# Kernel optimization log

Hardware: AMD Instinct MI355X
Metric: run time of the kernel (lower is better)

Reference implementation:

```python
import jax, jax.numpy as jnp
import numpy as np

EPS = 1e-8  # torch.nn.CosineSimilarity default eps


def setup_inputs() -> dict:
    key = jax.random.key(0)
    ks = jax.random.split(key, 7)
    B, T, D = 2048, 128, 128
    x = jax.random.normal(ks[0], (B, T, D), dtype=jnp.float32)
    def lin(k, fan_out, fan_in):
        kw, kb = jax.random.split(k)
        bound = 1.0 / np.sqrt(fan_in)
        W = jax.random.uniform(kw, (fan_out, fan_in), minval=-bound, maxval=bound, dtype=jnp.float32)
        b = jax.random.uniform(kb, (fan_out,), minval=-bound, maxval=bound, dtype=jnp.float32)
        return W, b
    W1, b1 = lin(ks[1], 96, 128)
    W2, b2 = lin(ks[2], 72, 96)
    W3, b3 = lin(ks[3], 64, 72)
    return {"x": x, "W1": W1, "b1": b1, "W2": W2, "b2": b2, "W3": W3, "b3": b3}


def reference(x, W1, b1, W2, b2, W3, b3):
    # Batched 3-layer MLP (equivalent to the per-slice Python loop).
    h = jax.nn.relu(jnp.einsum('btd,od->bto', x, W1) + b1)
    h = jax.nn.relu(jnp.einsum('bth,oh->bto', h, W2) + b2)
    f = jnp.einsum('bth,oh->bto', h, W3) + b3          # [B, T, 64]
    f = f.reshape(-1, f.shape[-1])                      # [N, 64], N = B*T
    n = jnp.maximum(jnp.linalg.norm(f, axis=-1, keepdims=True), EPS)
    u = f / n                                           # row-normalized feats
    # sum_{i<j} u_i . u_j = (||sum_i u_i||^2 - sum_i ||u_i||^2) / 2
    s = u.sum(axis=0)                                   # [64]
    pair_sum = 0.5 * (jnp.dot(s, s) - jnp.sum(u * u))
    return pair_sum / f.shape[0]
```

## Files before the change

kernel.cpp:

```cpp
#include <hip/hip_runtime.h>

typedef float  f32x4  __attribute__((ext_vector_type(4)));
typedef short  s16x8  __attribute__((ext_vector_type(8)));
typedef short  s16x4  __attribute__((ext_vector_type(4)));

#define NROWS (2048 * 128)
#define PASSES 8
#define HS 104
#define EPSF 1e-8f

union Frag { s16x8 v; unsigned short u[8]; };

__device__ __forceinline__ unsigned short f2bf(float f) {
    unsigned int u = __float_as_uint(f);
    u += 0x7fffu + ((u >> 16) & 1u);
    return (unsigned short)(u >> 16);
}

__global__ void repack(const float* __restrict__ W1, const float* __restrict__ b1,
                       const float* __restrict__ W2, const float* __restrict__ b2,
                       const float* __restrict__ W3, const float* __restrict__ b3,
                       unsigned short* __restrict__ w1f, unsigned short* __restrict__ w2f,
                       unsigned short* __restrict__ w3f,
                       float* __restrict__ b1p, float* __restrict__ b2p,
                       float* __restrict__ b3p)
{
    const int b = blockIdx.x;
    const int l = threadIdx.x;
    const int g = l >> 4, sl = l & 15;

    if (b < 24) {
        const int nt = b >> 2, ks = b & 3;
        const int o = nt * 16 + sl, kb = ks * 32 + g * 8;
        s16x8 v;
#pragma unroll
        for (int j = 0; j < 8; ++j) v[j] = (short)f2bf(W1[o * 128 + kb + j]);
        *(s16x8*)&w1f[b * 512 + l * 8] = v;
    } else if (b < 39) {
        const int f = b - 24, nt = f / 3, ks = f % 3;
        const int o = nt * 16 + sl, kb = ks * 32 + g * 8;
        s16x8 v;
#pragma unroll
        for (int j = 0; j < 8; ++j)
            v[j] = (short)((o < 72) ? f2bf(W2[o * 96 + kb + j]) : 0);
        *(s16x8*)&w2f[f * 512 + l * 8] = v;
    } else if (b < 51) {
        const int f = b - 39, nt = f / 3, ks = f % 3;
        const int o = nt * 16 + sl, kb = ks * 32 + g * 8;
        s16x8 v;
#pragma unroll
        for (int j = 0; j < 8; ++j)
            v[j] = (short)((kb + j < 72) ? f2bf(W3[o * 72 + kb + j]) : 0);
        *(s16x8*)&w3f[f * 512 + l * 8] = v;
    } else {
        for (int i = l; i < 240; i += 64) {
            if (i < 96)       b1p[i] = b1[i];
            else if (i < 176) { int o = i - 96; b2p[o] = (o < 72) ? b2[o] : 0.f; }
            else              b3p[i - 176] = b3[i - 176];
        }
    }
}

__global__ __launch_bounds__(256, 1)
void mlp_main(const float* __restrict__ x,
              const f32x4* __restrict__ w1src,
              const unsigned short* __restrict__ w2f,
              const unsigned short* __restrict__ w3f,
              float* __restrict__ acc )
{
    __shared__ __align__(16) unsigned char  wb[25536];
    __shared__ __align__(16) float          xbuf[4][2048];
    __shared__ __align__(16) unsigned short act[4][16][HS];
    __shared__ float sred[4][64];
    __shared__ float uured[4];

    const unsigned short* w1L = (const unsigned short*)wb;
    const float* b1L = (const float*)(wb + 24576);
    const float* b2L = b1L + 96;
    const float* b3L = b1L + 176;

    const int tid  = threadIdx.x;
    const int lane = tid & 63;
    const int wv   = tid >> 6;
    const int g    = lane >> 4;
    const int sl   = lane & 15;
    const int wave_gid = blockIdx.x * 4 + wv;

    auto stage = [&](int p) {
        const char* tb = (const char*)x
                       + ((size_t)wave_gid * 128 + (size_t)p * 16) * 512;
        float* dst = &xbuf[wv][0];
#pragma unroll
        for (int c = 0; c < 8; ++c) {
            const unsigned off = (unsigned)(c * 1024 + lane * 16);
            const unsigned so  = off ^ (((off >> 9) & 7u) << 4);
            __builtin_amdgcn_global_load_lds(
                (const __attribute__((address_space(1))) void*)(tb + so),
                (__attribute__((address_space(3))) void*)(dst + c * 256),
                16, 0, 0);
        }
    };

    stage(0);

    for (int i = tid; i < 1596; i += 256)
        ((f32x4*)wb)[i] = w1src[i];

    Frag W2r[5][3], W3r[4][3];
#pragma unroll
    for (int nt = 0; nt < 5; ++nt)
#pragma unroll
        for (int ks = 0; ks < 3; ++ks)
            W2r[nt][ks].v = *(const s16x8*)&w2f[(nt * 3 + ks) * 512 + lane * 8];
#pragma unroll
    for (int nt = 0; nt < 4; ++nt)
#pragma unroll
        for (int ks = 0; ks < 3; ++ks)
            W3r[nt][ks].v = *(const s16x8*)&w3f[(nt * 3 + ks) * 512 + lane * 8];

    __syncthreads();

    float uu_part = 0.f;
    float s_part[4] = {0.f, 0.f, 0.f, 0.f};

#pragma unroll 1
    for (int p = 0; p < PASSES; ++p) {
        asm volatile("s_waitcnt vmcnt(0)" ::: "memory");
        __builtin_amdgcn_sched_barrier(0);

        const char* xb = (const char*)&xbuf[wv][0];
        const unsigned sw = (unsigned)((sl & 7) << 4);
        f32x4 t[8];
#pragma unroll
        for (int ks = 0; ks < 4; ++ks)
#pragma unroll
            for (int h = 0; h < 2; ++h)
                t[ks * 2 + h] = *(const f32x4*)(
                    xb + sl * 512 + ks * 128 + (((unsigned)(g * 32 + h * 16)) ^ sw));
        Frag A1[4];
#pragma unroll
        for (int ks = 0; ks < 4; ++ks)
#pragma unroll
            for (int j = 0; j < 4; ++j) {
                A1[ks].u[j]     = f2bf(t[ks * 2 + 0][j]);
                A1[ks].u[4 + j] = f2bf(t[ks * 2 + 1][j]);
            }

        __builtin_amdgcn_sched_barrier(0);
        if (p + 1 < PASSES) stage(p + 1);

        f32x4 D1[6];
#pragma unroll
        for (int nt = 0; nt < 6; ++nt) {
            const float bb = b1L[nt * 16 + sl];
            D1[nt] = (f32x4){bb, bb, bb, bb};
        }
#pragma unroll
        for (int ks = 0; ks < 4; ++ks)
#pragma unroll
            for (int nt = 0; nt < 6; ++nt) {
                const s16x8 B = *(const s16x8*)&w1L[(nt * 4 + ks) * 512 + lane * 8];
                D1[nt] = __builtin_amdgcn_mfma_f32_16x16x32_bf16(A1[ks].v, B, D1[nt], 0, 0, 0);
            }
#pragma unroll
        for (int nt = 0; nt < 6; ++nt)
#pragma unroll
            for (int r = 0; r < 4; ++r)
                act[wv][g * 4 + r][nt * 16 + sl] = f2bf(fmaxf(D1[nt][r], 0.f));

        Frag A2[3];
#pragma unroll
        for (int ks = 0; ks < 3; ++ks)
            A2[ks].v = *(const s16x8*)&act[wv][sl][ks * 32 + g * 8];

        {
            const s16x4 z = (s16x4){0, 0, 0, 0};
            *(s16x4*)&act[wv][sl][80 + g * 4] = z;
        }

        f32x4 D2[5];
#pragma unroll
        for (int nt = 0; nt < 5; ++nt) {
            const float bb = b2L[nt * 16 + sl];
            D2[nt] = (f32x4){bb, bb, bb, bb};
        }
#pragma unroll
        for (int ks = 0; ks < 3; ++ks)
#pragma unroll
            for (int nt = 0; nt < 5; ++nt)
                D2[nt] = __builtin_amdgcn_mfma_f32_16x16x32_bf16(A2[ks].v, W2r[nt][ks].v, D2[nt], 0, 0, 0);
#pragma unroll
        for (int nt = 0; nt < 5; ++nt)
#pragma unroll
            for (int r = 0; r < 4; ++r)
                act[wv][g * 4 + r][nt * 16 + sl] = f2bf(fmaxf(D2[nt][r], 0.f));

        Frag A3[3];
#pragma unroll
        for (int ks = 0; ks < 3; ++ks)
            A3[ks].v = *(const s16x8*)&act[wv][sl][ks * 32 + g * 8];

        f32x4 D3[4];
#pragma unroll
        for (int nt = 0; nt < 4; ++nt) {
            const float bb = b3L[nt * 16 + sl];
            D3[nt] = (f32x4){bb, bb, bb, bb};
        }
#pragma unroll
        for (int ks = 0; ks < 3; ++ks)
#pragma unroll
            for (int nt = 0; nt < 4; ++nt)
                D3[nt] = __builtin_amdgcn_mfma_f32_16x16x32_bf16(A3[ks].v, W3r[nt][ks].v, D3[nt], 0, 0, 0);

        float ffr[4];
#pragma unroll
        for (int r = 0; r < 4; ++r) {
            float a = 0.f;
#pragma unroll
            for (int nt = 0; nt < 4; ++nt)
                a = fmaf(D3[nt][r], D3[nt][r], a);
            ffr[r] = a;
        }
#pragma unroll
        for (int r = 0; r < 4; ++r) {
            ffr[r] += __shfl_xor(ffr[r], 1, 64);
            ffr[r] += __shfl_xor(ffr[r], 2, 64);
            ffr[r] += __shfl_xor(ffr[r], 4, 64);
            ffr[r] += __shfl_xor(ffr[r], 8, 64);
        }
        float inv[4];
#pragma unroll
        for (int r = 0; r < 4; ++r) {
            inv[r] = 1.f / fmaxf(sqrtf(ffr[r]), EPSF);
            uu_part = fmaf(ffr[r] * inv[r], inv[r], uu_part);
        }
#pragma unroll
        for (int nt = 0; nt < 4; ++nt)
#pragma unroll
            for (int r = 0; r < 4; ++r)
                s_part[nt] = fmaf(D3[nt][r], inv[r], s_part[nt]);
    }

#pragma unroll
    for (int nt = 0; nt < 4; ++nt) {
        s_part[nt] += __shfl_xor(s_part[nt], 16, 64);
        s_part[nt] += __shfl_xor(s_part[nt], 32, 64);
    }
    uu_part += __shfl_xor(uu_part, 16, 64);
    uu_part += __shfl_xor(uu_part, 32, 64);

    if (g == 0) {
#pragma unroll
        for (int nt = 0; nt < 4; ++nt) sred[wv][nt * 16 + sl] = s_part[nt];
    }
    if (lane == 0) uured[wv] = uu_part * 0.0625f;
    __syncthreads();

    if (tid < 64) {
        const float t = sred[0][tid] + sred[1][tid] + sred[2][tid] + sred[3][tid];
        atomicAdd(&acc[tid], t);
    }
    if (tid == 0)
        atomicAdd(&acc[64], uured[0] + uured[1] + uured[2] + uured[3]);
}

__global__ void finalize_k(const float* __restrict__ acc, float* __restrict__ out)
{
    float s = acc[threadIdx.x];
    float d = s * s;
#pragma unroll
    for (int off = 32; off > 0; off >>= 1)
        d += __shfl_xor(d, off, 64);
    if (threadIdx.x == 0)
        out[0] = 0.5f * (d - acc[64]) / (float)NROWS;
}

extern "C" void kernel_launch(void* const* d_in, const int* in_sizes, int n_in,
                              void* d_out, int out_size, void* d_ws, size_t ws_size,
                              hipStream_t stream)
{
    const float* x  = (const float*)d_in[0];
    const float* W1 = (const float*)d_in[1];
    const float* b1 = (const float*)d_in[2];
    const float* W2 = (const float*)d_in[3];
    const float* b2 = (const float*)d_in[4];
    const float* W3 = (const float*)d_in[5];
    const float* b3 = (const float*)d_in[6];

    char* ws = (char*)d_ws;
    float*          acc = (float*)ws;
    unsigned short* w1f = (unsigned short*)(ws + 1024);
    float*          b1p = (float*)(ws + 25600);
    float*          b2p = (float*)(ws + 25984);
    float*          b3p = (float*)(ws + 26304);
    unsigned short* w2f = (unsigned short*)(ws + 26560);
    unsigned short* w3f = (unsigned short*)(ws + 41920);

    hipMemsetAsync(acc, 0, 1024, stream);
    repack<<<52, 64, 0, stream>>>(W1, b1, W2, b2, W3, b3, w1f, w2f, w3f, b1p, b2p, b3p);
    mlp_main<<<NROWS / (4 * PASSES * 16), 256, 0, stream>>>(
        x, (const f32x4*)(ws + 1024), w2f, w3f, acc);
    finalize_k<<<1, 64, 0, stream>>>(acc, (float*)d_out);
}
```

Before: 54.91 us.

## Swap MFMA operands so features land along rows, vectorize activation stores

Computes the transposed product (weights as A, activations as B) in all three MLP layers, so each lane holds four consecutive feature columns of one row. Activation writeback to LDS becomes one 8-byte store per tile instead of four scalar 2-byte stores, and biases load as f32x4. The per-row norm reduction shrinks from four 16-lane shuffle trees to two cross-group shuffles and a single rsqrt per lane. In exchange, the column-sum accumulators grow to 16 registers per lane and need a larger shuffle reduction after the loop.

```diff
diff --git a/kernel.cpp b/kernel.cpp
--- a/kernel.cpp
+++ b/kernel.cpp
@@ -84,6 +84,7 @@
     const int wv   = tid >> 6;
     const int g    = lane >> 4;
     const int sl   = lane & 15;
+    const int g4   = g * 4;
     const int wave_gid = blockIdx.x * 4 + wv;
 
     auto stage = [&](int p) {
@@ -121,7 +122,11 @@
     __syncthreads();
 
     float uu_part = 0.f;
-    float s_part[4] = {0.f, 0.f, 0.f, 0.f};
+    float s_part[4][4];
+#pragma unroll
+    for (int nt = 0; nt < 4; ++nt)
+#pragma unroll
+        for (int r = 0; r < 4; ++r) s_part[nt][r] = 0.f;
 
 #pragma unroll 1
     for (int p = 0; p < PASSES; ++p) {
@@ -137,13 +142,13 @@
             for (int h = 0; h < 2; ++h)
                 t[ks * 2 + h] = *(const f32x4*)(
                     xb + sl * 512 + ks * 128 + (((unsigned)(g * 32 + h * 16)) ^ sw));
-        Frag A1[4];
+        Frag X1[4];
 #pragma unroll
         for (int ks = 0; ks < 4; ++ks)
 #pragma unroll
             for (int j = 0; j < 4; ++j) {
-                A1[ks].u[j]     = f2bf(t[ks * 2 + 0][j]);
-                A1[ks].u[4 + j] = f2bf(t[ks * 2 + 1][j]);
+                X1[ks].u[j]     = f2bf(t[ks * 2 + 0][j]);
+                X1[ks].u[4 + j] = f2bf(t[ks * 2 + 1][j]);
             }
 
         __builtin_amdgcn_sched_barrier(0);
@@ -151,22 +156,22 @@
 
         f32x4 D1[6];
 #pragma unroll
+        for (int nt = 0; nt < 6; ++nt)
+            D1[nt] = *(const f32x4*)&b1L[nt * 16 + g4];
+#pragma unroll
+        for (int ks = 0; ks < 4; ++ks)
+#pragma unroll
+            for (int nt = 0; nt < 6; ++nt) {
+                const s16x8 Wf = *(const s16x8*)&w1L[(nt * 4 + ks) * 512 + lane * 8];
+                D1[nt] = __builtin_amdgcn_mfma_f32_16x16x32_bf16(Wf, X1[ks].v, D1[nt], 0, 0, 0);
+            }
+#pragma unroll
         for (int nt = 0; nt < 6; ++nt) {
-            const float bb = b1L[nt * 16 + sl];
-            D1[nt] = (f32x4){bb, bb, bb, bb};
-        }
-#pragma unroll
-        for (int ks = 0; ks < 4; ++ks)
-#pragma unroll
-            for (int nt = 0; nt < 6; ++nt) {
-                const s16x8 B = *(const s16x8*)&w1L[(nt * 4 + ks) * 512 + lane * 8];
-                D1[nt] = __builtin_amdgcn_mfma_f32_16x16x32_bf16(A1[ks].v, B, D1[nt], 0, 0, 0);
-            }
-#pragma unroll
-        for (int nt = 0; nt < 6; ++nt)
-#pragma unroll
-            for (int r = 0; r < 4; ++r)
-                act[wv][g * 4 + r][nt * 16 + sl] = f2bf(fmaxf(D1[nt][r], 0.f));
+            s16x4 q;
+#pragma unroll
+            for (int j = 0; j < 4; ++j) q[j] = (short)f2bf(fmaxf(D1[nt][j], 0.f));
+            *(s16x4*)&act[wv][sl][nt * 16 + g4] = q;
+        }
 
         Frag A2[3];
 #pragma unroll
@@ -175,90 +180,84 @@
 
         {
             const s16x4 z = (s16x4){0, 0, 0, 0};
-            *(s16x4*)&act[wv][sl][80 + g * 4] = z;
+            *(s16x4*)&act[wv][sl][80 + g4] = z;
         }
 
         f32x4 D2[5];
 #pragma unroll
+        for (int nt = 0; nt < 5; ++nt)
+            D2[nt] = *(const f32x4*)&b2L[nt * 16 + g4];
+#pragma unroll
+        for (int ks = 0; ks < 3; ++ks)
+#pragma unroll
+            for (int nt = 0; nt < 5; ++nt)
+                D2[nt] = __builtin_amdgcn_mfma_f32_16x16x32_bf16(W2r[nt][ks].v, A2[ks].v, D2[nt], 0, 0, 0);
+#pragma unroll
         for (int nt = 0; nt < 5; ++nt) {
-            const float bb = b2L[nt * 16 + sl];
-            D2[nt] = (f32x4){bb, bb, bb, bb};
-        }
-#pragma unroll
-        for (int ks = 0; ks < 3; ++ks)
-#pragma unroll
-            for (int nt = 0; nt < 5; ++nt)
-                D2[nt] = __builtin_amdgcn_mfma_f32_16x16x32_bf16(A2[ks].v, W2r[nt][ks].v, D2[nt], 0, 0, 0);
-#pragma unroll
-        for (int nt = 0; nt < 5; ++nt)
+            s16x4 q;
+#pragma unroll
+            for (int j = 0; j < 4; ++j) q[j] = (short)f2bf(fmaxf(D2[nt][j], 0.f));
+            *(s16x4*)&act[wv][sl][nt * 16 + g4] = q;
+        }
+
+        Frag A3[3];
+#pragma unroll
+        for (int ks = 0; ks < 3; ++ks)
+            A3[ks].v = *(const s16x8*)&act[wv][sl][ks * 32 + g * 8];
+
+        f32x4 D3[4];
+#pragma unroll
+        for (int nt = 0; nt < 4; ++nt)
+            D3[nt] = *(const f32x4*)&b3L[nt * 16 + g4];
+#pragma unroll
+        for (int ks = 0; ks < 3; ++ks)
+#pragma unroll
+            for (int nt = 0; nt < 4; ++nt)
+                D3[nt] = __builtin_amdgcn_mfma_f32_16x16x32_bf16(W3r[nt][ks].v, A3[ks].v, D3[nt], 0, 0, 0);
+
+        float ff = 0.f;
+#pragma unroll
+        for (int nt = 0; nt < 4; ++nt)
 #pragma unroll
             for (int r = 0; r < 4; ++r)
-                act[wv][g * 4 + r][nt * 16 + sl] = f2bf(fmaxf(D2[nt][r], 0.f));
-
-        Frag A3[3];
-#pragma unroll
-        for (int ks = 0; ks < 3; ++ks)
-            A3[ks].v = *(const s16x8*)&act[wv][sl][ks * 32 + g * 8];
-
-        f32x4 D3[4];
+                ff = fmaf(D3[nt][r], D3[nt][r], ff);
+        ff += __shfl_xor(ff, 16, 64);
+        ff += __shfl_xor(ff, 32, 64);
+        const float inv = 1.f / fmaxf(sqrtf(ff), EPSF);
+        uu_part = fmaf(ff * inv, inv, uu_part);
+#pragma unroll
+        for (int nt = 0; nt < 4; ++nt)
+#pragma unroll
+            for (int r = 0; r < 4; ++r)
+                s_part[nt][r] = fmaf(D3[nt][r], inv, s_part[nt][r]);
+    }
+
+#pragma unroll
+    for (int nt = 0; nt < 4; ++nt)
+#pragma unroll
+        for (int r = 0; r < 4; ++r) {
+            s_part[nt][r] += __shfl_xor(s_part[nt][r], 1, 64);
+            s_part[nt][r] += __shfl_xor(s_part[nt][r], 2, 64);
+            s_part[nt][r] += __shfl_xor(s_part[nt][r], 4, 64);
+            s_part[nt][r] += __shfl_xor(s_part[nt][r], 8, 64);
+        }
+#pragma unroll
+    for (int off = 1; off < 64; off <<= 1)
+        uu_part += __shfl_xor(uu_part, off, 64);
+
+    if (sl == 0) {
 #pragma unroll
         for (int nt = 0; nt < 4; ++nt) {
-            const float bb = b3L[nt * 16 + sl];
-            D3[nt] = (f32x4){bb, bb, bb, bb};
-        }
-#pragma unroll
-        for (int ks = 0; ks < 3; ++ks)
-#pragma unroll
-            for (int nt = 0; nt < 4; ++nt)
-                D3[nt] = __builtin_amdgcn_mfma_f32_16x16x32_bf16(A3[ks].v, W3r[nt][ks].v, D3[nt], 0, 0, 0);
-
-        float ffr[4];
-#pragma unroll
-        for (int r = 0; r < 4; ++r) {
-            float a = 0.f;
-#pragma unroll
-            for (int nt = 0; nt < 4; ++nt)
-                a = fmaf(D3[nt][r], D3[nt][r], a);
-            ffr[r] = a;
-        }
-#pragma unroll
-        for (int r = 0; r < 4; ++r) {
-            ffr[r] += __shfl_xor(ffr[r], 1, 64);
-            ffr[r] += __shfl_xor(ffr[r], 2, 64);
-            ffr[r] += __shfl_xor(ffr[r], 4, 64);
-            ffr[r] += __shfl_xor(ffr[r], 8, 64);
-        }
-        float inv[4];
-#pragma unroll
-        for (int r = 0; r < 4; ++r) {
-            inv[r] = 1.f / fmaxf(sqrtf(ffr[r]), EPSF);
-            uu_part = fmaf(ffr[r] * inv[r], inv[r], uu_part);
-        }
-#pragma unroll
-        for (int nt = 0; nt < 4; ++nt)
-#pragma unroll
-            for (int r = 0; r < 4; ++r)
-                s_part[nt] = fmaf(D3[nt][r], inv[r], s_part[nt]);
+            f32x4 v = {s_part[nt][0], s_part[nt][1], s_part[nt][2], s_part[nt][3]};
+            *(f32x4*)&sred[wv][nt * 16 + g4] = v;
+        }
     }
-
-#pragma unroll
-    for (int nt = 0; nt < 4; ++nt) {
-        s_part[nt] += __shfl_xor(s_part[nt], 16, 64);
-        s_part[nt] += __shfl_xor(s_part[nt], 32, 64);
-    }
-    uu_part += __shfl_xor(uu_part, 16, 64);
-    uu_part += __shfl_xor(uu_part, 32, 64);
-
-    if (g == 0) {
-#pragma unroll
-        for (int nt = 0; nt < 4; ++nt) sred[wv][nt * 16 + sl] = s_part[nt];
-    }
-    if (lane == 0) uured[wv] = uu_part * 0.0625f;
+    if (lane == 0) uured[wv] = uu_part * 0.25f;
     __syncthreads();
 
     if (tid < 64) {
-        const float t = sred[0][tid] + sred[1][tid] + sred[2][tid] + sred[3][tid];
-        atomicAdd(&acc[tid], t);
+        const float t2 = sred[0][tid] + sred[1][tid] + sred[2][tid] + sred[3][tid];
+        atomicAdd(&acc[tid], t2);
     }
     if (tid == 0)
         atomicAdd(&acc[64], uured[0] + uured[1] + uured[2] + uured[3]);
```

Result: faster. 53.18 us (-3.1%).
